# Performance work log

Hardware: AMD Instinct MI355X
Metric: run time of the kernel (lower is better)

The kernel has to match this reference:

```python
import jax, jax.numpy as jnp
import numpy as np

DIM = 3072          # model dim
H = 24              # num heads (q == kv heads here)
DH = 128            # head dim
EPS = 1e-6
SCALE = 1.0 / float(np.sqrt(DH))
S_IMG, S_TXT, B = 2048, 256, 1


def _rmsnorm(x, w):
    # per-head RMSNorm over last (head_dim) axis
    return x * jax.lax.rsqrt(jnp.mean(x * x, axis=-1, keepdims=True) + EPS) * w


def _rope_non_neox(x, cos, sin):
    # x: [B,S,H,DH]; cos/sin: [S,DH/2]; interleaved (non-neox) rotation
    x1 = x[..., 0::2]
    x2 = x[..., 1::2]
    c = cos[None, :, None, :]
    s = sin[None, :, None, :]
    o1 = x1 * c - x2 * s
    o2 = x2 * c + x1 * s
    return jnp.stack([o1, o2], axis=-1).reshape(x.shape)


def setup_inputs() -> dict:
    key = jax.random.key(0)
    ks = jax.random.split(key, 16)
    hidden_states = jax.random.normal(ks[0], (B, S_IMG, DIM), jnp.float32)
    encoder_hidden_states = jax.random.normal(ks[1], (B, S_TXT, DIM), jnp.float32)
    vid_ang = jax.random.uniform(ks[2], (S_IMG, DH // 2), jnp.float32) * (2 * np.pi)
    txt_ang = jax.random.uniform(ks[3], (S_TXT, DH // 2), jnp.float32) * (2 * np.pi)
    w = 0.02
    return {
        "hidden_states": hidden_states,
        "encoder_hidden_states": encoder_hidden_states,
        "vid_cos": jnp.cos(vid_ang), "vid_sin": jnp.sin(vid_ang),
        "txt_cos": jnp.cos(txt_ang), "txt_sin": jnp.sin(txt_ang),
        "w_qkv": jax.random.normal(ks[4], (DIM, 3 * H * DH), jnp.float32) * w,
        "b_qkv": jnp.zeros((3 * H * DH,), jnp.float32),
        "w_add_qkv": jax.random.normal(ks[5], (DIM, 3 * H * DH), jnp.float32) * w,
        "b_add_qkv": jnp.zeros((3 * H * DH,), jnp.float32),
        "norm_q_w": jnp.ones((DH,), jnp.float32),
        "norm_k_w": jnp.ones((DH,), jnp.float32),
        "norm_aq_w": jnp.ones((DH,), jnp.float32),
        "norm_ak_w": jnp.ones((DH,), jnp.float32),
        "w_out": jax.random.normal(ks[6], (H * DH, DIM), jnp.float32) * w,
        "b_out": jnp.zeros((DIM,), jnp.float32),
        "w_add_out": jax.random.normal(ks[7], (H * DH, DIM), jnp.float32) * w,
        "b_add_out": jnp.zeros((DIM,), jnp.float32),
    }


def reference(hidden_states, encoder_hidden_states, vid_cos, vid_sin,
              txt_cos, txt_sin, w_qkv, b_qkv, w_add_qkv, b_add_qkv,
              norm_q_w, norm_k_w, norm_aq_w, norm_ak_w,
              w_out, b_out, w_add_out, b_add_out):
    qs = H * DH
    # fused QKV projections
    img_qkv = hidden_states @ w_qkv + b_qkv                  # [B,Si,3*H*DH]
    txt_qkv = encoder_hidden_states @ w_add_qkv + b_add_qkv  # [B,St,3*H*DH]

    def split_heads(qkv, S):
        q, k, v = qkv[..., :qs], qkv[..., qs:2 * qs], qkv[..., 2 * qs:]
        shp = (qkv.shape[0], S, H, DH)
        return q.reshape(shp), k.reshape(shp), v.reshape(shp)

    img_q, img_k, img_v = split_heads(img_qkv, S_IMG)
    txt_q, txt_k, txt_v = split_heads(txt_qkv, S_TXT)

    # per-head RMSNorm on q/k
    img_q = _rmsnorm(img_q, norm_q_w)
    img_k = _rmsnorm(img_k, norm_k_w)
    txt_q = _rmsnorm(txt_q, norm_aq_w)
    txt_k = _rmsnorm(txt_k, norm_ak_w)

    # non-neox RoPE on both query and key
    img_q = _rope_non_neox(img_q, vid_cos, vid_sin)
    img_k = _rope_non_neox(img_k, vid_cos, vid_sin)
    txt_q = _rope_non_neox(txt_q, txt_cos, txt_sin)
    txt_k = _rope_non_neox(txt_k, txt_cos, txt_sin)

    # joint text|image attention (text first), non-causal SDPA
    q = jnp.concatenate([txt_q, img_q], axis=1)  # [B,S,H,DH]
    k = jnp.concatenate([txt_k, img_k], axis=1)
    v = jnp.concatenate([txt_v, img_v], axis=1)

    scores = jnp.einsum('bqhd,bkhd->bhqk', q, k) * SCALE
    probs = jax.nn.softmax(scores, axis=-1)
    attn = jnp.einsum('bhqk,bkhd->bqhd', probs, v)           # [B,S,H,DH]
    attn = attn.reshape(attn.shape[0], attn.shape[1], H * DH)

    txt_attn = attn[:, :S_TXT, :]
    img_attn = attn[:, S_TXT:, :]
    img_out = img_attn @ w_out + b_out
    txt_out = txt_attn @ w_add_out + b_add_out
    return (img_out, txt_out)
```

## Files before the change

### kernel.cpp

```cpp
#include <hip/hip_runtime.h>

typedef unsigned short u16;
typedef __attribute__((ext_vector_type(8))) short bf16x8;
typedef __attribute__((ext_vector_type(4))) float f32x4;
typedef __attribute__((ext_vector_type(16))) float f32x16;

#define H_    24
#define DH_   128
#define DIM_  3072
#define NQKV_ 9216
#define SIMG_ 2048
#define STXT_ 256
#define SQ_   2304
#define SL_   0.1275258646912204f

__device__ __forceinline__ float bf2f(u16 h) {
  union { unsigned u; float f; } x; x.u = ((unsigned)h) << 16; return x.f;
}
__device__ __forceinline__ u16 f2bf(float f) {
  union { float f; unsigned u; } x; x.f = f;
  unsigned r = x.u + 0x7FFFu + ((x.u >> 16) & 1u);
  return (u16)(r >> 16);
}
__device__ __forceinline__ unsigned cvt_pk_bf16(float lo, float hi) {
  unsigned r;
  asm("v_cvt_pk_bf16_f32 %0, %1, %2" : "=v"(r) : "v"(lo), "v"(hi));
  return r;
}

__device__ __forceinline__ void gld16(const u16* g, u16* l) {
  __builtin_amdgcn_global_load_lds(
      (const __attribute__((address_space(1))) unsigned*)g,
      (__attribute__((address_space(3))) unsigned*)l, 16, 0, 0);
}

__global__ __launch_bounds__(256) void k_f2b2(const float* __restrict__ in0,
                                              u16* __restrict__ out0, int n0,
                                              const float* __restrict__ in1,
                                              u16* __restrict__ out1, int n1) {
  int i = (blockIdx.x * 256 + threadIdx.x) * 4;
  const float* in = in0;
  u16* out = out0;
  int n = n0;
  if (i >= n0) { i -= n0; in = in1; out = out1; n = n1; }
  if (i < n) {
    float4 v = *(const float4*)(in + i);
    ushort4 o;
    o.x = f2bf(v.x); o.y = f2bf(v.y); o.z = f2bf(v.z); o.w = f2bf(v.w);
    *(ushort4*)(out + i) = o;
  }
}

__global__ __launch_bounds__(256) void k_transpose2(const float* __restrict__ in0,
                                                    u16* __restrict__ out0,
                                                    const float* __restrict__ in1,
                                                    u16* __restrict__ out1,
                                                    int R, int C) {
  __shared__ __align__(16) u16 tile[64][72];
  const float* in = blockIdx.z ? in1 : in0;
  u16* out = blockIdx.z ? out1 : out0;
  const int t = threadIdx.x;
  const int tx = t & 15, ty = t >> 4;
  const int bc = blockIdx.x * 64, br = blockIdx.y * 64;
#pragma unroll
  for (int i = 0; i < 4; ++i) {
    const int r = ty + i * 16;
    float4 v = *(const float4*)(in + (size_t)(br + r) * C + bc + tx * 4);
    ushort4 o;
    o.x = f2bf(v.x); o.y = f2bf(v.y); o.z = f2bf(v.z); o.w = f2bf(v.w);
    *(ushort4*)&tile[r][tx * 4] = o;
  }
  __syncthreads();
#pragma unroll
  for (int i = 0; i < 4; ++i) {
    const int c = ty + i * 16;
    ushort4 v;
    v.x = tile[tx * 4 + 0][c];
    v.y = tile[tx * 4 + 1][c];
    v.z = tile[tx * 4 + 2][c];
    v.w = tile[tx * 4 + 3][c];
    *(ushort4*)(out + (size_t)(bc + c) * R + br + tx * 4) = v;
  }
}

template <bool F32OUT>
__global__ __launch_bounds__(256) void k_gemm_bt2(const u16* __restrict__ A0,
                                                  const u16* __restrict__ Bt0,
                                                  const float* __restrict__ bias0,
                                                  void* __restrict__ C0,
                                                  int M0,
                                                  const u16* __restrict__ A1,
                                                  const u16* __restrict__ Bt1,
                                                  const float* __restrict__ bias1,
                                                  void* __restrict__ C1,
                                                  int M1,
                                                  int N, int K, int nblk0) {
  __shared__ __align__(16) u16 As[2][128 * 32];
  __shared__ __align__(16) u16 Bs[2][128 * 32];
  const int t = threadIdx.x, w = t >> 6, l = t & 63;
  const int lr = l & 15, lg = l >> 4;
  const int wr = w >> 1, wc = w & 1;

  const u16 *A, *Bt;
  const float* bias;
  void* Cv;
  int M, wg, nwg;
  if ((int)blockIdx.x < nblk0) {
    A = A0; Bt = Bt0; bias = bias0; Cv = C0; M = M0;
    wg = blockIdx.x; nwg = nblk0;
  } else {
    A = A1; Bt = Bt1; bias = bias1; Cv = C1; M = M1;
    wg = blockIdx.x - nblk0; nwg = gridDim.x - nblk0;
  }
  const int nbm = M >> 7;
  if ((nwg & 7) == 0) {
    const int c = nwg >> 3;
    wg = (wg & 7) * c + (wg >> 3);
  }
  const int bm = (wg % nbm) * 128, bn = (wg / nbm) * 128;

  f32x4 acc[4][4];
#pragma unroll
  for (int i = 0; i < 4; ++i)
#pragma unroll
    for (int j = 0; j < 4; ++j) acc[i][j] = (f32x4){0.f, 0.f, 0.f, 0.f};

  const u16* Ag = A + (size_t)(bm + (t >> 2)) * K + (t & 3) * 8;
  const u16* Bg = Bt + (size_t)(bn + (t >> 2)) * K + (t & 3) * 8;

#define GSTAGE(buf)                                        \
  do {                                                     \
    gld16(Ag, &As[buf][t * 8]);                            \
    gld16(Ag + (size_t)64 * K, &As[buf][t * 8 + 2048]);    \
    gld16(Bg, &Bs[buf][t * 8]);                            \
    gld16(Bg + (size_t)64 * K, &Bs[buf][t * 8 + 2048]);    \
    Ag += 32; Bg += 32;                                    \
  } while (0)

  GSTAGE(0);
  const int nt = K >> 5;
  for (int tile = 0; tile < nt; ++tile) {
    const int cur = tile & 1;
    if (tile + 1 < nt) {
      GSTAGE(cur ^ 1);
      asm volatile("s_waitcnt vmcnt(4)" ::: "memory");
    } else {
      asm volatile("s_waitcnt vmcnt(0)" ::: "memory");
    }
    __builtin_amdgcn_s_barrier();
    bf16x8 af[4], bfr[4];
#pragma unroll
    for (int i = 0; i < 4; ++i)
      af[i] = *(const bf16x8*)&As[cur][(wr * 64 + i * 16 + lr) * 32 + lg * 8];
#pragma unroll
    for (int j = 0; j < 4; ++j)
      bfr[j] = *(const bf16x8*)&Bs[cur][(wc * 64 + j * 16 + lr) * 32 + lg * 8];
#pragma unroll
    for (int i = 0; i < 4; ++i)
#pragma unroll
      for (int j = 0; j < 4; ++j)
        acc[i][j] = __builtin_amdgcn_mfma_f32_16x16x32_bf16(af[i], bfr[j], acc[i][j], 0, 0, 0);
    __builtin_amdgcn_s_barrier();
  }
#undef GSTAGE

#pragma unroll
  for (int j = 0; j < 4; ++j) {
    const int col = bn + wc * 64 + j * 16 + lr;
    const float bv = bias[col];
#pragma unroll
    for (int i = 0; i < 4; ++i) {
      const int row = bm + wr * 64 + i * 16 + lg * 4;
#pragma unroll
      for (int r = 0; r < 4; ++r) {
        const float v = acc[i][j][r] + bv;
        if constexpr (F32OUT)
          ((float*)Cv)[(size_t)(row + r) * N + col] = v;
        else
          ((u16*)Cv)[(size_t)(row + r) * N + col] = f2bf(v);
      }
    }
  }
}

__global__ __launch_bounds__(256) void k_norm_rope(
    const u16* __restrict__ img_qkv, const u16* __restrict__ txt_qkv,
    const float* __restrict__ vid_cos, const float* __restrict__ vid_sin,
    const float* __restrict__ txt_cos, const float* __restrict__ txt_sin,
    const float* __restrict__ nq, const float* __restrict__ nk,
    const float* __restrict__ naq, const float* __restrict__ nak,
    u16* __restrict__ Qb, u16* __restrict__ Kb) {
  const int wid = blockIdx.x * 4 + (threadIdx.x >> 6);
  const int lane = threadIdx.x & 63;
  const int h = wid % H_, s = wid / H_;

  const u16* src;
  const float *cp, *sp, *qw, *kw;
  if (s < STXT_) {
    src = txt_qkv + (size_t)s * NQKV_;
    cp = txt_cos + s * 64; sp = txt_sin + s * 64;
    qw = naq; kw = nak;
  } else {
    const int si = s - STXT_;
    src = img_qkv + (size_t)si * NQKV_;
    cp = vid_cos + si * 64; sp = vid_sin + si * 64;
    qw = nq; kw = nk;
  }
  const float c = cp[lane], sn = sp[lane];
  const size_t drow = ((size_t)h * SQ_ + s) * DH_;

  {
    ushort2 p = *(const ushort2*)(src + h * DH_ + 2 * lane);
    float x1 = bf2f(p.x), x2 = bf2f(p.y);
    float ss = x1 * x1 + x2 * x2;
#pragma unroll
    for (int m = 1; m < 64; m <<= 1) ss += __shfl_xor(ss, m);
    const float rr = rsqrtf(ss * (1.0f / 128.0f) + 1e-6f);
    const float xn1 = x1 * rr * qw[2 * lane];
    const float xn2 = x2 * rr * qw[2 * lane + 1];
    ushort2 o; o.x = f2bf(xn1 * c - xn2 * sn); o.y = f2bf(xn2 * c + xn1 * sn);
    *(ushort2*)(Qb + drow + 2 * lane) = o;
  }
  {
    ushort2 p = *(const ushort2*)(src + DIM_ + h * DH_ + 2 * lane);
    float x1 = bf2f(p.x), x2 = bf2f(p.y);
    float ss = x1 * x1 + x2 * x2;
#pragma unroll
    for (int m = 1; m < 64; m <<= 1) ss += __shfl_xor(ss, m);
    const float rr = rsqrtf(ss * (1.0f / 128.0f) + 1e-6f);
    const float xn1 = x1 * rr * kw[2 * lane];
    const float xn2 = x2 * rr * kw[2 * lane + 1];
    ushort2 o; o.x = f2bf(xn1 * c - xn2 * sn); o.y = f2bf(xn2 * c + xn1 * sn);
    const int col = (2 * lane) ^ ((s & 7) << 3);
    *(ushort2*)(Kb + drow + col) = o;
  }
}

__global__ __launch_bounds__(256) void k_vt(const u16* __restrict__ img_qkv,
                                            const u16* __restrict__ txt_qkv,
                                            u16* __restrict__ Vt) {
  __shared__ __align__(16) u16 tile[64][136];
  const int h = blockIdx.y, sb = blockIdx.x;
  const int t = threadIdx.x;
  {
    const int row = t >> 2, cc = (t & 3) * 32;
    const int s = sb * 64 + row;
    const u16* src = (s < STXT_) ? (txt_qkv + (size_t)s * NQKV_)
                                 : (img_qkv + (size_t)(s - STXT_) * NQKV_);
    src += 2 * DIM_ + h * DH_ + cc;
#pragma unroll
    for (int u = 0; u < 4; ++u) {
      uint4 a = *(const uint4*)(src + u * 8);
      *(uint4*)&tile[row][cc + u * 8] = a;
    }
  }
  __syncthreads();
  {
    const int w = t >> 6, lane = t & 63;
#pragma unroll 4
    for (int dd = 0; dd < 32; ++dd) {
      const int d = w * 32 + dd;
      const int m = (d & 7) << 3;
      const u16 v = tile[lane][d];
      Vt[((size_t)h * DH_ + d) * SQ_ + sb * 64 + (lane ^ m)] = v;
    }
  }
}

__global__ __launch_bounds__(256, 2) void k_attn(const u16* __restrict__ Qb,
                                                 const u16* __restrict__ Kb,
                                                 const u16* __restrict__ Vt,
                                                 u16* __restrict__ attnb) {
  __shared__ __align__(16) u16 Ks[2][64 * 128];
  __shared__ __align__(16) u16 Vs[2][128 * 64];
  const int t = threadIdx.x, w = t >> 6, l = t & 63;
  const int lo = l & 31, hi = l >> 5;

  const int bid = blockIdx.x;
  const int xcd = bid & 7, jj = bid >> 3;
  const int h = xcd * 3 + jj / 18;
  const int qb = jj % 18;

  const int q0 = qb * 128 + w * 32;
  const size_t head = (size_t)h * SQ_ * DH_;

  bf16x8 qf[8];
  {
    const u16* qp = Qb + head + (size_t)(q0 + lo) * DH_ + hi * 8;
#pragma unroll
    for (int ks = 0; ks < 8; ++ks) qf[ks] = *(const bf16x8*)(qp + ks * 16);
  }
  f32x16 oacc[4];
#pragma unroll
  for (int dt = 0; dt < 4; ++dt)
#pragma unroll
    for (int i = 0; i < 16; ++i) oacc[dt][i] = 0.f;
  float mrun = -1e30f, lrun = 0.f;

  const u16* kg0 = Kb + head + (size_t)(t >> 4) * DH_ + (t & 15) * 8;
  const u16* vg0 = Vt + head + (size_t)(t >> 3) * SQ_ + (t & 7) * 8;
  const int swz = (lo & 7) << 3;

#define STAGE(buf, kt)                                                   \
  do {                                                                   \
    const u16* kg_ = kg0 + (size_t)(kt) * 64 * DH_;                      \
    _Pragma("unroll")                                                    \
    for (int r_ = 0; r_ < 4; ++r_)                                       \
      gld16(kg_ + (size_t)r_ * 16 * DH_, &Ks[buf][t * 8 + r_ * 2048]);   \
    const u16* vg_ = vg0 + (kt) * 64;                                    \
    _Pragma("unroll")                                                    \
    for (int r_ = 0; r_ < 4; ++r_)                                       \
      gld16(vg_ + (size_t)r_ * 32 * SQ_, &Vs[buf][t * 8 + r_ * 2048]);   \
  } while (0)

  STAGE(0, 0);
  const int nt = SQ_ / 64;
  for (int kt = 0; kt < nt; ++kt) {
    const int cur = kt & 1;
    if (kt + 1 < nt) {
      STAGE(cur ^ 1, kt + 1);
      asm volatile("s_waitcnt vmcnt(8)" ::: "memory");
    } else {
      asm volatile("s_waitcnt vmcnt(0)" ::: "memory");
    }
    __builtin_amdgcn_s_barrier();

    f32x16 sv0, sv1;
#pragma unroll
    for (int i = 0; i < 16; ++i) { sv0[i] = 0.f; sv1[i] = 0.f; }
#pragma unroll
    for (int ks = 0; ks < 8; ++ks) {
      bf16x8 kf = *(const bf16x8*)&Ks[cur][lo * DH_ + ((ks * 16 + hi * 8) ^ swz)];
      sv0 = __builtin_amdgcn_mfma_f32_32x32x16_bf16(kf, qf[ks], sv0, 0, 0, 0);
    }
#pragma unroll
    for (int ks = 0; ks < 8; ++ks) {
      bf16x8 kf = *(const bf16x8*)&Ks[cur][(32 + lo) * DH_ + ((ks * 16 + hi * 8) ^ swz)];
      sv1 = __builtin_amdgcn_mfma_f32_32x32x16_bf16(kf, qf[ks], sv1, 0, 0, 0);
    }

    float tm = sv0[0];
#pragma unroll
    for (int i = 1; i < 16; ++i) tm = fmaxf(tm, sv0[i]);
#pragma unroll
    for (int i = 0; i < 16; ++i) tm = fmaxf(tm, sv1[i]);
    tm = fmaxf(tm, __shfl_xor(tm, 32));
    const float sc = tm * SL_;
    if (!__all(sc - mrun <= 8.0f)) {
      const float mn = fmaxf(mrun, sc);
      const float scl = __builtin_amdgcn_exp2f(mrun - mn);
      mrun = mn;
      lrun *= scl;
#pragma unroll
      for (int dt = 0; dt < 4; ++dt)
#pragma unroll
        for (int i = 0; i < 16; ++i) oacc[dt][i] *= scl;
    }
    float p0[16], p1[16];
    float rs = 0.f;
#pragma unroll
    for (int i = 0; i < 16; ++i) {
      p0[i] = __builtin_amdgcn_exp2f(fmaf(sv0[i], SL_, -mrun));
      rs += p0[i];
    }
#pragma unroll
    for (int i = 0; i < 16; ++i) {
      p1[i] = __builtin_amdgcn_exp2f(fmaf(sv1[i], SL_, -mrun));
      rs += p1[i];
    }
    rs += __shfl_xor(rs, 32);
    lrun += rs;

    unsigned xx[16];
#pragma unroll
    for (int g = 0; g < 8; ++g) xx[g] = cvt_pk_bf16(p0[2 * g], p0[2 * g + 1]);
#pragma unroll
    for (int g = 0; g < 8; ++g) xx[8 + g] = cvt_pk_bf16(p1[2 * g], p1[2 * g + 1]);
#pragma unroll
    for (int b = 0; b < 16; b += 4) {
      asm("v_permlane32_swap_b32 %0, %1" : "+v"(xx[b]), "+v"(xx[b + 2]));
      asm("v_permlane32_swap_b32 %0, %1" : "+v"(xx[b + 1]), "+v"(xx[b + 3]));
    }
    bf16x8 pb[4];
#pragma unroll
    for (int st = 0; st < 4; ++st) {
      union { unsigned u[4]; bf16x8 b; } cv;
      cv.u[0] = xx[4 * st]; cv.u[1] = xx[4 * st + 1];
      cv.u[2] = xx[4 * st + 2]; cv.u[3] = xx[4 * st + 3];
      pb[st] = cv.b;
    }

#pragma unroll
    for (int dt = 0; dt < 4; ++dt) {
      const int drow = dt * 32 + lo;
#pragma unroll
      for (int st = 0; st < 4; ++st) {
        bf16x8 vf = *(const bf16x8*)&Vs[cur][drow * 64 + ((st * 16 + hi * 8) ^ swz)];
        oacc[dt] = __builtin_amdgcn_mfma_f32_32x32x16_bf16(vf, pb[st], oacc[dt], 0, 0, 0);
      }
    }
    __builtin_amdgcn_s_barrier();
  }
#undef STAGE

  const float rinv = 1.0f / lrun;
  u16* op = attnb + (size_t)(q0 + lo) * DIM_ + h * DH_ + hi * 4;
#pragma unroll
  for (int dt = 0; dt < 4; ++dt)
#pragma unroll
    for (int g = 0; g < 4; ++g) {
      uint2 u;
      u.x = cvt_pk_bf16(oacc[dt][4 * g + 0] * rinv, oacc[dt][4 * g + 1] * rinv);
      u.y = cvt_pk_bf16(oacc[dt][4 * g + 2] * rinv, oacc[dt][4 * g + 3] * rinv);
      *(uint2*)(op + dt * 32 + g * 8) = u;
    }
}

extern "C" void kernel_launch(void* const* d_in, const int* in_sizes, int n_in,
                              void* d_out, int out_size, void* d_ws, size_t ws_size,
                              hipStream_t stream) {
  (void)in_sizes; (void)n_in; (void)out_size; (void)ws_size;
  const float* hidden    = (const float*)d_in[0];
  const float* encoder   = (const float*)d_in[1];
  const float* vid_cos   = (const float*)d_in[2];
  const float* vid_sin   = (const float*)d_in[3];
  const float* txt_cos   = (const float*)d_in[4];
  const float* txt_sin   = (const float*)d_in[5];
  const float* w_qkv     = (const float*)d_in[6];
  const float* b_qkv     = (const float*)d_in[7];
  const float* w_add_qkv = (const float*)d_in[8];
  const float* b_add_qkv = (const float*)d_in[9];
  const float* norm_q_w  = (const float*)d_in[10];
  const float* norm_k_w  = (const float*)d_in[11];
  const float* norm_aq_w = (const float*)d_in[12];
  const float* norm_ak_w = (const float*)d_in[13];
  const float* w_out     = (const float*)d_in[14];
  const float* b_out     = (const float*)d_in[15];
  const float* w_add_out = (const float*)d_in[16];
  const float* b_add_out = (const float*)d_in[17];
  float* out = (float*)d_out;

  char* ws = (char*)d_ws;
  u16* wqkv_t    = (u16*)(ws + 0);
  u16* waddqkv_t = (u16*)(ws + 56623104);
  u16* img_qkv   = (u16*)(ws + 113246208);
  u16* txt_qkv   = (u16*)(ws + 150994944);
  u16* Qb        = (u16*)(ws + 155713536);
  u16* Kb        = (u16*)(ws + 169869312);
  u16* Vt        = (u16*)(ws + 184025088);
  u16* wout_t    = wqkv_t;
  u16* waddout_t = waddqkv_t;
  u16* attnb     = img_qkv;
  u16* hidden_bf = Qb;
  u16* encoder_bf = Kb;

  k_f2b2<<<(SIMG_ * DIM_ + STXT_ * DIM_) / 1024, 256, 0, stream>>>(
      hidden, hidden_bf, SIMG_ * DIM_, encoder, encoder_bf, STXT_ * DIM_);
  k_transpose2<<<dim3(NQKV_ / 64, DIM_ / 64, 2), 256, 0, stream>>>(
      w_qkv, wqkv_t, w_add_qkv, waddqkv_t, DIM_, NQKV_);
  k_gemm_bt2<false><<<(SIMG_ / 128 + STXT_ / 128) * (NQKV_ / 128), 256, 0, stream>>>(
      hidden_bf, wqkv_t, b_qkv, img_qkv, SIMG_,
      encoder_bf, waddqkv_t, b_add_qkv, txt_qkv, STXT_,
      NQKV_, DIM_, (SIMG_ / 128) * (NQKV_ / 128));
  k_norm_rope<<<(SQ_ * H_) / 4, 256, 0, stream>>>(img_qkv, txt_qkv, vid_cos, vid_sin,
                                                  txt_cos, txt_sin, norm_q_w, norm_k_w,
                                                  norm_aq_w, norm_ak_w, Qb, Kb);
  k_vt<<<dim3(SQ_ / 64, H_), 256, 0, stream>>>(img_qkv, txt_qkv, Vt);
  k_attn<<<(SQ_ / 128) * H_, 256, 0, stream>>>(Qb, Kb, Vt, attnb);
  k_transpose2<<<dim3(DIM_ / 64, DIM_ / 64, 2), 256, 0, stream>>>(
      w_out, wout_t, w_add_out, waddout_t, DIM_, DIM_);
  k_gemm_bt2<true><<<(SIMG_ / 128 + STXT_ / 128) * (DIM_ / 128), 256, 0, stream>>>(
      attnb + (size_t)STXT_ * DIM_, wout_t, b_out, out, SIMG_,
      attnb, waddout_t, b_add_out, out + (size_t)SIMG_ * DIM_, STXT_,
      DIM_, DIM_, (SIMG_ / 128) * (DIM_ / 128));
}
```

Baseline: 439.2 us.

## Fuse QK RMSNorm, RoPE and V transpose into QKV GEMM epilogue

The QKV projection GEMM now applies bias, per-head RMSNorm and interleaved RoPE to Q and K inside its epilogue and writes them straight into the attention layouts, and writes V directly in transposed, swizzled form. Because each 128-wide N tile is exactly one head, the row sum of squares is reduced across lanes and across the two column warps through a small shared buffer. This drops the intermediate bf16 QKV buffers and the separate norm/rope and V-transpose kernels, saving a round trip through global memory and two launches. In exchange the epilogue does scattered 2-byte stores and strided cos/sin loads, which may write less efficiently than the old dedicated kernels.

```diff
diff --git a/kernel.cpp b/kernel.cpp
--- a/kernel.cpp
+++ b/kernel.cpp
@@ -80,6 +80,180 @@
     v.z = tile[tx * 4 + 2][c];
     v.w = tile[tx * 4 + 3][c];
     *(ushort4*)(out + (size_t)(bc + c) * R + br + tx * 4) = v;
+  }
+}
+
+__global__ __launch_bounds__(256) void k_gemm_qkv(
+    const u16* __restrict__ A0, const u16* __restrict__ Bt0,
+    const float* __restrict__ bias0, int M0,
+    const u16* __restrict__ A1, const u16* __restrict__ Bt1,
+    const float* __restrict__ bias1, int M1,
+    const float* __restrict__ vcos, const float* __restrict__ vsin,
+    const float* __restrict__ tcos, const float* __restrict__ tsin,
+    const float* __restrict__ nq0, const float* __restrict__ nk0,
+    const float* __restrict__ nq1, const float* __restrict__ nk1,
+    u16* __restrict__ Qb, u16* __restrict__ Kb, u16* __restrict__ Vt,
+    int K, int nblk0) {
+  __shared__ __align__(16) u16 As[2][128 * 32];
+  __shared__ __align__(16) u16 Bs[2][128 * 32];
+  __shared__ float rbuf[2][128];
+  const int t = threadIdx.x, w = t >> 6, l = t & 63;
+  const int lr = l & 15, lg = l >> 4;
+  const int wr = w >> 1, wc = w & 1;
+  const int N = NQKV_;
+
+  const u16 *A, *Bt;
+  const float *bias, *cosp, *sinp, *wq, *wk;
+  int M, wg, nwg, sbase;
+  if ((int)blockIdx.x < nblk0) {
+    A = A0; Bt = Bt0; bias = bias0; M = M0;
+    cosp = vcos; sinp = vsin; wq = nq0; wk = nk0; sbase = STXT_;
+    wg = blockIdx.x; nwg = nblk0;
+  } else {
+    A = A1; Bt = Bt1; bias = bias1; M = M1;
+    cosp = tcos; sinp = tsin; wq = nq1; wk = nk1; sbase = 0;
+    wg = blockIdx.x - nblk0; nwg = gridDim.x - nblk0;
+  }
+  const int nbm = M >> 7;
+  if ((nwg & 7) == 0) {
+    const int c = nwg >> 3;
+    wg = (wg & 7) * c + (wg >> 3);
+  }
+  const int bm = (wg % nbm) * 128, bn = (wg / nbm) * 128;
+
+  f32x4 acc[4][4];
+#pragma unroll
+  for (int i = 0; i < 4; ++i)
+#pragma unroll
+    for (int j = 0; j < 4; ++j) acc[i][j] = (f32x4){0.f, 0.f, 0.f, 0.f};
+
+  const u16* Ag = A + (size_t)(bm + (t >> 2)) * K + (t & 3) * 8;
+  const u16* Bg = Bt + (size_t)(bn + (t >> 2)) * K + (t & 3) * 8;
+
+#define GSTAGE(buf)                                        \
+  do {                                                     \
+    gld16(Ag, &As[buf][t * 8]);                            \
+    gld16(Ag + (size_t)64 * K, &As[buf][t * 8 + 2048]);    \
+    gld16(Bg, &Bs[buf][t * 8]);                            \
+    gld16(Bg + (size_t)64 * K, &Bs[buf][t * 8 + 2048]);    \
+    Ag += 32; Bg += 32;                                    \
+  } while (0)
+
+  GSTAGE(0);
+  const int nt = K >> 5;
+  for (int tile = 0; tile < nt; ++tile) {
+    const int cur = tile & 1;
+    if (tile + 1 < nt) {
+      GSTAGE(cur ^ 1);
+      asm volatile("s_waitcnt vmcnt(4)" ::: "memory");
+    } else {
+      asm volatile("s_waitcnt vmcnt(0)" ::: "memory");
+    }
+    __builtin_amdgcn_s_barrier();
+    bf16x8 af[4], bfr[4];
+#pragma unroll
+    for (int i = 0; i < 4; ++i)
+      af[i] = *(const bf16x8*)&As[cur][(wr * 64 + i * 16 + lr) * 32 + lg * 8];
+#pragma unroll
+    for (int j = 0; j < 4; ++j)
+      bfr[j] = *(const bf16x8*)&Bs[cur][(wc * 64 + j * 16 + lr) * 32 + lg * 8];
+#pragma unroll
+    for (int i = 0; i < 4; ++i)
+#pragma unroll
+      for (int j = 0; j < 4; ++j)
+        acc[i][j] = __builtin_amdgcn_mfma_f32_16x16x32_bf16(af[i], bfr[j], acc[i][j], 0, 0, 0);
+    __builtin_amdgcn_s_barrier();
+  }
+#undef GSTAGE
+
+  const int seg = bn / 3072;
+  const int hh = (bn % 3072) >> 7;
+  (void)N;
+  float bj[4];
+#pragma unroll
+  for (int j = 0; j < 4; ++j) bj[j] = bias[bn + wc * 64 + j * 16 + lr];
+#pragma unroll
+  for (int i = 0; i < 4; ++i)
+#pragma unroll
+    for (int j = 0; j < 4; ++j)
+#pragma unroll
+      for (int r = 0; r < 4; ++r) acc[i][j][r] += bj[j];
+
+  if (seg == 2) {
+#pragma unroll
+    for (int i = 0; i < 4; ++i) {
+      const int s4 = sbase + bm + wr * 64 + i * 16 + lg * 4;
+#pragma unroll
+      for (int j = 0; j < 4; ++j) {
+        const int d = wc * 64 + j * 16 + lr;
+        const int sw = (s4 & ~63) | ((s4 & 63) ^ ((d & 7) << 3));
+        ushort4 o;
+        o.x = f2bf(acc[i][j][0]); o.y = f2bf(acc[i][j][1]);
+        o.z = f2bf(acc[i][j][2]); o.w = f2bf(acc[i][j][3]);
+        *(ushort4*)(Vt + (size_t)(hh * DH_ + d) * SQ_ + sw) = o;
+      }
+    }
+  } else {
+    float ss[4][4];
+#pragma unroll
+    for (int i = 0; i < 4; ++i)
+#pragma unroll
+      for (int r = 0; r < 4; ++r) {
+        float s = 0.f;
+#pragma unroll
+        for (int j = 0; j < 4; ++j) s += acc[i][j][r] * acc[i][j][r];
+        ss[i][r] = s;
+      }
+#pragma unroll
+    for (int m = 1; m < 16; m <<= 1)
+#pragma unroll
+      for (int i = 0; i < 4; ++i)
+#pragma unroll
+        for (int r = 0; r < 4; ++r) ss[i][r] += __shfl_xor(ss[i][r], m);
+    if (lr == 0) {
+#pragma unroll
+      for (int i = 0; i < 4; ++i)
+#pragma unroll
+        for (int r = 0; r < 4; ++r)
+          rbuf[wc][wr * 64 + i * 16 + lg * 4 + r] = ss[i][r];
+    }
+    __syncthreads();
+    float rr[4][4];
+#pragma unroll
+    for (int i = 0; i < 4; ++i)
+#pragma unroll
+      for (int r = 0; r < 4; ++r) {
+        const float tot = ss[i][r] + rbuf[wc ^ 1][wr * 64 + i * 16 + lg * 4 + r];
+        rr[i][r] = rsqrtf(tot * (1.0f / 128.0f) + 1e-6f);
+      }
+    const float* wn = (seg == 0) ? wq : wk;
+    float wj[4];
+#pragma unroll
+    for (int j = 0; j < 4; ++j) wj[j] = wn[wc * 64 + j * 16 + lr];
+    const float sgn = (l & 1) ? 1.f : -1.f;
+#pragma unroll
+    for (int i = 0; i < 4; ++i)
+#pragma unroll
+      for (int r = 0; r < 4; ++r) {
+        const int lrow = wr * 64 + i * 16 + lg * 4 + r;
+        const int srow = bm + lrow;
+        const float* cr = cosp + (size_t)srow * 64;
+        const float* sr = sinp + (size_t)srow * 64;
+        const int sg = sbase + srow;
+#pragma unroll
+        for (int j = 0; j < 4; ++j) {
+          const int d = wc * 64 + j * 16 + lr;
+          const float x = acc[i][j][r] * rr[i][r] * wj[j];
+          const float part = __shfl_xor(x, 1);
+          const int dp = d >> 1;
+          const float o = x * cr[dp] + sgn * part * sr[dp];
+          const u16 ob = f2bf(o);
+          if (seg == 0)
+            Qb[((size_t)hh * SQ_ + sg) * DH_ + d] = ob;
+          else
+            Kb[((size_t)hh * SQ_ + sg) * DH_ + (d ^ ((sg & 7) << 3))] = ob;
+        }
+      }
   }
 }
 
@@ -179,90 +353,6 @@
         else
           ((u16*)Cv)[(size_t)(row + r) * N + col] = f2bf(v);
       }
-    }
-  }
-}
-
-__global__ __launch_bounds__(256) void k_norm_rope(
-    const u16* __restrict__ img_qkv, const u16* __restrict__ txt_qkv,
-    const float* __restrict__ vid_cos, const float* __restrict__ vid_sin,
-    const float* __restrict__ txt_cos, const float* __restrict__ txt_sin,
-    const float* __restrict__ nq, const float* __restrict__ nk,
-    const float* __restrict__ naq, const float* __restrict__ nak,
-    u16* __restrict__ Qb, u16* __restrict__ Kb) {
-  const int wid = blockIdx.x * 4 + (threadIdx.x >> 6);
-  const int lane = threadIdx.x & 63;
-  const int h = wid % H_, s = wid / H_;
-
-  const u16* src;
-  const float *cp, *sp, *qw, *kw;
-  if (s < STXT_) {
-    src = txt_qkv + (size_t)s * NQKV_;
-    cp = txt_cos + s * 64; sp = txt_sin + s * 64;
-    qw = naq; kw = nak;
-  } else {
-    const int si = s - STXT_;
-    src = img_qkv + (size_t)si * NQKV_;
-    cp = vid_cos + si * 64; sp = vid_sin + si * 64;
-    qw = nq; kw = nk;
-  }
-  const float c = cp[lane], sn = sp[lane];
-  const size_t drow = ((size_t)h * SQ_ + s) * DH_;
-
-  {
-    ushort2 p = *(const ushort2*)(src + h * DH_ + 2 * lane);
-    float x1 = bf2f(p.x), x2 = bf2f(p.y);
-    float ss = x1 * x1 + x2 * x2;
-#pragma unroll
-    for (int m = 1; m < 64; m <<= 1) ss += __shfl_xor(ss, m);
-    const float rr = rsqrtf(ss * (1.0f / 128.0f) + 1e-6f);
-    const float xn1 = x1 * rr * qw[2 * lane];
-    const float xn2 = x2 * rr * qw[2 * lane + 1];
-    ushort2 o; o.x = f2bf(xn1 * c - xn2 * sn); o.y = f2bf(xn2 * c + xn1 * sn);
-    *(ushort2*)(Qb + drow + 2 * lane) = o;
-  }
-  {
-    ushort2 p = *(const ushort2*)(src + DIM_ + h * DH_ + 2 * lane);
-    float x1 = bf2f(p.x), x2 = bf2f(p.y);
-    float ss = x1 * x1 + x2 * x2;
-#pragma unroll
-    for (int m = 1; m < 64; m <<= 1) ss += __shfl_xor(ss, m);
-    const float rr = rsqrtf(ss * (1.0f / 128.0f) + 1e-6f);
-    const float xn1 = x1 * rr * kw[2 * lane];
-    const float xn2 = x2 * rr * kw[2 * lane + 1];
-    ushort2 o; o.x = f2bf(xn1 * c - xn2 * sn); o.y = f2bf(xn2 * c + xn1 * sn);
-    const int col = (2 * lane) ^ ((s & 7) << 3);
-    *(ushort2*)(Kb + drow + col) = o;
-  }
-}
-
-__global__ __launch_bounds__(256) void k_vt(const u16* __restrict__ img_qkv,
-                                            const u16* __restrict__ txt_qkv,
-                                            u16* __restrict__ Vt) {
-  __shared__ __align__(16) u16 tile[64][136];
-  const int h = blockIdx.y, sb = blockIdx.x;
-  const int t = threadIdx.x;
-  {
-    const int row = t >> 2, cc = (t & 3) * 32;
-    const int s = sb * 64 + row;
-    const u16* src = (s < STXT_) ? (txt_qkv + (size_t)s * NQKV_)
-                                 : (img_qkv + (size_t)(s - STXT_) * NQKV_);
-    src += 2 * DIM_ + h * DH_ + cc;
-#pragma unroll
-    for (int u = 0; u < 4; ++u) {
-      uint4 a = *(const uint4*)(src + u * 8);
-      *(uint4*)&tile[row][cc + u * 8] = a;
-    }
-  }
-  __syncthreads();
-  {
-    const int w = t >> 6, lane = t & 63;
-#pragma unroll 4
-    for (int dd = 0; dd < 32; ++dd) {
-      const int d = w * 32 + dd;
-      const int m = (d & 7) << 3;
-      const u16 v = tile[lane][d];
-      Vt[((size_t)h * DH_ + d) * SQ_ + sb * 64 + (lane ^ m)] = v;
     }
   }
 }
@@ -441,31 +531,27 @@
   float* out = (float*)d_out;
 
   char* ws = (char*)d_ws;
-  u16* wqkv_t    = (u16*)(ws + 0);
-  u16* waddqkv_t = (u16*)(ws + 56623104);
-  u16* img_qkv   = (u16*)(ws + 113246208);
-  u16* txt_qkv   = (u16*)(ws + 150994944);
-  u16* Qb        = (u16*)(ws + 155713536);
-  u16* Kb        = (u16*)(ws + 169869312);
-  u16* Vt        = (u16*)(ws + 184025088);
-  u16* wout_t    = wqkv_t;
-  u16* waddout_t = waddqkv_t;
-  u16* attnb     = img_qkv;
-  u16* hidden_bf = Qb;
-  u16* encoder_bf = Kb;
+  u16* wqkv_t     = (u16*)(ws + 0);
+  u16* waddqkv_t  = (u16*)(ws + 56623104);
+  u16* hidden_bf  = (u16*)(ws + 113246208);
+  u16* encoder_bf = (u16*)(ws + 125829120);
+  u16* attnb      = (u16*)(ws + 113246208);
+  u16* Qb         = (u16*)(ws + 155713536);
+  u16* Kb         = (u16*)(ws + 169869312);
+  u16* Vt         = (u16*)(ws + 184025088);
+  u16* wout_t     = wqkv_t;
+  u16* waddout_t  = waddqkv_t;
 
   k_f2b2<<<(SIMG_ * DIM_ + STXT_ * DIM_) / 1024, 256, 0, stream>>>(
       hidden, hidden_bf, SIMG_ * DIM_, encoder, encoder_bf, STXT_ * DIM_);
   k_transpose2<<<dim3(NQKV_ / 64, DIM_ / 64, 2), 256, 0, stream>>>(
       w_qkv, wqkv_t, w_add_qkv, waddqkv_t, DIM_, NQKV_);
-  k_gemm_bt2<false><<<(SIMG_ / 128 + STXT_ / 128) * (NQKV_ / 128), 256, 0, stream>>>(
-      hidden_bf, wqkv_t, b_qkv, img_qkv, SIMG_,
-      encoder_bf, waddqkv_t, b_add_qkv, txt_qkv, STXT_,
-      NQKV_, DIM_, (SIMG_ / 128) * (NQKV_ / 128));
-  k_norm_rope<<<(SQ_ * H_) / 4, 256, 0, stream>>>(img_qkv, txt_qkv, vid_cos, vid_sin,
-                                                  txt_cos, txt_sin, norm_q_w, norm_k_w,
-                                                  norm_aq_w, norm_ak_w, Qb, Kb);
-  k_vt<<<dim3(SQ_ / 64, H_), 256, 0, stream>>>(img_qkv, txt_qkv, Vt);
+  k_gemm_qkv<<<(SIMG_ / 128 + STXT_ / 128) * (NQKV_ / 128), 256, 0, stream>>>(
+      hidden_bf, wqkv_t, b_qkv, SIMG_,
+      encoder_bf, waddqkv_t, b_add_qkv, STXT_,
+      vid_cos, vid_sin, txt_cos, txt_sin,
+      norm_q_w, norm_k_w, norm_aq_w, norm_ak_w,
+      Qb, Kb, Vt, DIM_, (SIMG_ / 128) * (NQKV_ / 128));
   k_attn<<<(SQ_ / 128) * H_, 256, 0, stream>>>(Qb, Kb, Vt, attnb);
   k_transpose2<<<dim3(DIM_ / 64, DIM_ / 64, 2), 256, 0, stream>>>(
       w_out, wout_t, w_add_out, waddout_t, DIM_, DIM_);
```

Result: slower. 492.0 us (+12.0%).
